# Optimization experiments

Measured on AMD Instinct MI355X. Metric: run time of the kernel, lower is better.

Reference implementation:

```python
import jax, jax.numpy as jnp
import numpy as np

N_NODES = 10000
N_EDGES = 640000
IN_FEATS = 256
H_FEATS = 128
NUM_CLASSES = 64


def _kaiming(key, shape):
    fan_in = shape[1]
    std = np.sqrt(2.0 / fan_in)
    return jax.random.normal(key, shape, dtype=jnp.float32) * std


def setup_inputs() -> dict:
    key = jax.random.key(0)
    ks = jax.random.split(key, 10)
    x = jax.random.normal(ks[0], (N_NODES, IN_FEATS), dtype=jnp.float32)
    edge_index = jax.random.randint(ks[1], (2, N_EDGES), 0, N_NODES, dtype=jnp.int64)
    return {
        "x": x,
        "edge_index": edge_index,
        "W_lin": _kaiming(ks[2], (H_FEATS, IN_FEATS)),
        "b_lin": jnp.zeros((H_FEATS,), jnp.float32),
        "Wl1": _kaiming(ks[3], (H_FEATS, H_FEATS)),
        "bl1": jnp.zeros((H_FEATS,), jnp.float32),
        "Wr1": _kaiming(ks[4], (H_FEATS, H_FEATS)),
        "Wl2": _kaiming(ks[5], (H_FEATS, H_FEATS)),
        "bl2": jnp.zeros((H_FEATS,), jnp.float32),
        "Wr2": _kaiming(ks[6], (H_FEATS, H_FEATS)),
        "W_cls": _kaiming(ks[7], (NUM_CLASSES, H_FEATS)),
    }


def _sage_conv(x, src, dst, Wl, bl, Wr, n_nodes):
    # PyG SAGEConv (mean aggr): out = lin_l(mean_{j->i} x_j) + lin_r(x_i)
    msg = x[src]                                    # [E, H] gather
    agg = jax.ops.segment_sum(msg, dst, num_segments=n_nodes)  # [N, H]
    deg = jax.ops.segment_sum(jnp.ones((src.shape[0],), x.dtype), dst,
                              num_segments=n_nodes)            # [N]
    mean = agg / jnp.maximum(deg, 1.0)[:, None]
    return mean @ Wl.T + bl + x @ Wr.T


def reference(x, edge_index, W_lin, b_lin, Wl1, bl1, Wr1, Wl2, bl2, Wr2, W_cls):
    src, dst = edge_index[0], edge_index[1]
    n = x.shape[0]
    h = jax.nn.relu(x @ W_lin.T + b_lin)            # input projection + relu
    h = _sage_conv(h, src, dst, Wl1, bl1, Wr1, n)   # sage1 (no relu: linear is truthy)
    h = _sage_conv(h, src, dst, Wl2, bl2, Wr2, n)   # sage2
    h = jax.nn.relu(h)
    return h @ W_cls.T                              # weight.mm(x.t()).t()
```

## Files before the change

### kernel.cpp

```cpp
#include <hip/hip_runtime.h>

#define NN 10000
#define HF 128
#define INF_ 256
#define CLS 64
#define NR 8
#define SEG 32
#define CAPT (NR * SEG)
#define NP 10240
#define RT  (NN / 16)
#define LDP (HF + 8)

typedef __attribute__((ext_vector_type(8))) short short8;
typedef __attribute__((ext_vector_type(4))) float f32x4;

__device__ __forceinline__ unsigned short f2bf(float f) {
    unsigned u = __builtin_bit_cast(unsigned, f);
    u = (u + 0x7fffu + ((u >> 16) & 1u)) >> 16;
    return (unsigned short)u;
}
__device__ __forceinline__ float bfbits2f(unsigned u) {
    u <<= 16;
    return __builtin_bit_cast(float, u);
}


template <int K, int NC>
__device__ __forceinline__
void mfma_cols(int row_tile, int col0,
               const unsigned short* __restrict__ A, int lda,
               const unsigned short* __restrict__ W, f32x4* acc) {
    int lane = threadIdx.x & 63;
    int m = lane & 15, quad = lane >> 4;
    const unsigned short* arow = A + (size_t)(row_tile * 16 + m) * lda + quad * 8;
    const short8* bp[NC];
#pragma unroll
    for (int c = 0; c < NC; ++c)
        bp[c] = (const short8*)(W + (size_t)(col0 + c * 16 + m) * K + quad * 8);
#pragma unroll
    for (int k0 = 0; k0 < K; k0 += 32) {
        short8 a = *(const short8*)(arow + k0);
#pragma unroll
        for (int c = 0; c < NC; ++c)
            acc[c] = __builtin_amdgcn_mfma_f32_16x16x32_bf16(a, bp[c][k0 >> 3], acc[c], 0, 0, 0);
    }
}

template <int NC, bool OUT_BF16, bool RELU_OUT, bool HAS_BIAS>
__device__ __forceinline__
void epilogue_n(int row_tile, int col0, int N, const float* __restrict__ bias,
                f32x4* acc, void* __restrict__ out) {
    int lane = threadIdx.x & 63;
    int m = lane & 15, quad = lane >> 4;
#pragma unroll
    for (int c = 0; c < NC; ++c) {
        int colg = col0 + c * 16 + m;
        float bv = HAS_BIAS ? bias[colg] : 0.f;
#pragma unroll
        for (int r = 0; r < 4; ++r) {
            int rowg = row_tile * 16 + quad * 4 + r;
            float v = acc[c][r] + bv;
            if (RELU_OUT) v = fmaxf(v, 0.f);
            if (OUT_BF16) ((unsigned short*)out)[(size_t)rowg * N + colg] = f2bf(v);
            else          ((float*)out)[(size_t)rowg * N + colg] = v;
        }
    }
}

__device__ __forceinline__ short8 pack8(float4 a, float4 b) {
    short8 r;
    r[0] = (short)f2bf(a.x); r[1] = (short)f2bf(a.y);
    r[2] = (short)f2bf(a.z); r[3] = (short)f2bf(a.w);
    r[4] = (short)f2bf(b.x); r[5] = (short)f2bf(b.y);
    r[6] = (short)f2bf(b.z); r[7] = (short)f2bf(b.w);
    return r;
}

__device__ __forceinline__
void gemm1_wave(int row_tile, int col0, const float* __restrict__ x,
                const float* __restrict__ Wlin, const float* __restrict__ blin,
                unsigned short* __restrict__ h0) {
    int lane = threadIdx.x & 63;
    int m = lane & 15, quad = lane >> 4;
    const float* ar = x    + (size_t)(row_tile * 16 + m) * INF_ + quad * 8;
    const float* w0 = Wlin + (size_t)(col0 +  0 + m) * INF_ + quad * 8;
    const float* w1 = Wlin + (size_t)(col0 + 16 + m) * INF_ + quad * 8;
    const float* w2 = Wlin + (size_t)(col0 + 32 + m) * INF_ + quad * 8;
    const float* w3 = Wlin + (size_t)(col0 + 48 + m) * INF_ + quad * 8;
    f32x4 acc[4] = {};
#pragma unroll
    for (int k0 = 0; k0 < INF_; k0 += 32) {
        short8 a  = pack8(*(const float4*)(ar + k0), *(const float4*)(ar + k0 + 4));
        short8 b0 = pack8(*(const float4*)(w0 + k0), *(const float4*)(w0 + k0 + 4));
        short8 b1 = pack8(*(const float4*)(w1 + k0), *(const float4*)(w1 + k0 + 4));
        short8 b2 = pack8(*(const float4*)(w2 + k0), *(const float4*)(w2 + k0 + 4));
        short8 b3 = pack8(*(const float4*)(w3 + k0), *(const float4*)(w3 + k0 + 4));
        acc[0] = __builtin_amdgcn_mfma_f32_16x16x32_bf16(a, b0, acc[0], 0, 0, 0);
        acc[1] = __builtin_amdgcn_mfma_f32_16x16x32_bf16(a, b1, acc[1], 0, 0, 0);
        acc[2] = __builtin_amdgcn_mfma_f32_16x16x32_bf16(a, b2, acc[2], 0, 0, 0);
        acc[3] = __builtin_amdgcn_mfma_f32_16x16x32_bf16(a, b3, acc[3], 0, 0, 0);
    }
    epilogue_n<4, true, true, true>(row_tile, col0, HF, blin, acc, h0);
}

#define GB 313
#define FB 2500
#define CB 288

__global__ __launch_bounds__(256)
void fused_k(const float* __restrict__ x, const float* __restrict__ Wlin,
             const float* __restrict__ blin, unsigned short* __restrict__ h0,
             const int* __restrict__ src, const int* __restrict__ dst,
             int* __restrict__ cnt8, unsigned short* __restrict__ colb, int E,
             const float* __restrict__ Wl1, const float* __restrict__ Wr1,
             const float* __restrict__ Wl2, const float* __restrict__ Wr2,
             const float* __restrict__ Wcls, unsigned short* __restrict__ wb) {
    int b = blockIdx.x;
    if (b < GB) {
        int wave = threadIdx.x >> 6;
        int row_tile = b * 2 + (wave >> 1);
        if (row_tile >= RT) return;
        gemm1_wave(row_tile, (wave & 1) * 64, x, Wlin, blin, h0);
    } else if (b < GB + FB) {
        int r = b & 7;
        int i = (b - GB) * 256 + threadIdx.x;
        if (i < E) {
            int d = dst[i];
            int pos = atomicAdd(&cnt8[r * NP + d], 1);
            if (pos < SEG) colb[(size_t)d * CAPT + r * SEG + pos] = (unsigned short)src[i];
        }
    } else {
        int i = (b - GB - FB) * 256 + threadIdx.x;
        const float* s; int off;
        if      (i < 16384) { s = Wl1;  off = 0; }
        else if (i < 32768) { s = Wr1;  off = 16384; }
        else if (i < 49152) { s = Wl2;  off = 32768; }
        else if (i < 65536) { s = Wr2;  off = 49152; }
        else if (i < 73728) { s = Wcls; off = 65536; }
        else return;
        wb[i] = f2bf(s[i - off]);
    }
}

__device__ __forceinline__
void gather_mean(const unsigned short* __restrict__ h,
                 const int* __restrict__ cnt8, int node,
                 const unsigned short* __restrict__ seg,
                 unsigned short* __restrict__ cols,
                 unsigned short* __restrict__ msrow) {
    int lane = threadIdx.x & 63;
    int q   = lane >> 4;
    int r16 = lane & 15;

    int craw0 = 0;
    if (lane < 8) craw0 = cnt8[lane * NP + node];
    int c0 = craw0 > SEG ? SEG : craw0;
    int off0 = 0, deg = 0, cdeg = 0;
#pragma unroll
    for (int i = 0; i < 8; ++i) {
        int ci = __shfl(c0, i);
        int ri = __shfl(craw0, i);
        if (lane > i) off0 += ci;
        cdeg += ci;
        deg  += ri;
    }
#pragma unroll
    for (int p = 0; p < 4; ++p) {
        int r = 2 * p + (lane >> 5);
        int j = lane & 31;
        unsigned short v = seg[r * SEG + j];
        int cr  = __shfl(c0, r);
        int orr = __shfl(off0, r);
        if (j < cr) cols[orr + j] = v;
    }

    const uint4* __restrict__ hp = (const uint4*)h;
    float a0 = 0.f, a1 = 0.f, a2 = 0.f, a3 = 0.f;
    float a4 = 0.f, a5 = 0.f, a6 = 0.f, a7 = 0.f;
#pragma unroll 4
    for (int e0 = 0; e0 < cdeg; e0 += 4) {
        int e = e0 + q;
        if (e < cdeg) {
            int s = (int)cols[e];
            uint4 v = hp[(size_t)s * 16 + r16];
            a0 += bfbits2f(v.x & 0xffffu); a1 += bfbits2f(v.x >> 16);
            a2 += bfbits2f(v.y & 0xffffu); a3 += bfbits2f(v.y >> 16);
            a4 += bfbits2f(v.z & 0xffffu); a5 += bfbits2f(v.z >> 16);
            a6 += bfbits2f(v.w & 0xffffu); a7 += bfbits2f(v.w >> 16);
        }
    }
    a0 += __shfl_xor(a0, 16); a0 += __shfl_xor(a0, 32);
    a1 += __shfl_xor(a1, 16); a1 += __shfl_xor(a1, 32);
    a2 += __shfl_xor(a2, 16); a2 += __shfl_xor(a2, 32);
    a3 += __shfl_xor(a3, 16); a3 += __shfl_xor(a3, 32);
    a4 += __shfl_xor(a4, 16); a4 += __shfl_xor(a4, 32);
    a5 += __shfl_xor(a5, 16); a5 += __shfl_xor(a5, 32);
    a6 += __shfl_xor(a6, 16); a6 += __shfl_xor(a6, 32);
    a7 += __shfl_xor(a7, 16); a7 += __shfl_xor(a7, 32);
    if (q == 0) {
        float inv = (deg > 0) ? 1.0f / (float)deg : 0.f;
        uint4 o;
        o.x = (unsigned)f2bf(a0 * inv) | ((unsigned)f2bf(a1 * inv) << 16);
        o.y = (unsigned)f2bf(a2 * inv) | ((unsigned)f2bf(a3 * inv) << 16);
        o.z = (unsigned)f2bf(a4 * inv) | ((unsigned)f2bf(a5 * inv) << 16);
        o.w = (unsigned)f2bf(a6 * inv) | ((unsigned)f2bf(a7 * inv) << 16);
        ((uint4*)msrow)[r16] = o;
    }
}

__global__ __launch_bounds__(1024)
void aggfin1_k(const unsigned short* __restrict__ h0, const int* __restrict__ cnt8,
               const unsigned short* __restrict__ colb,
               const unsigned short* __restrict__ Wr, const unsigned short* __restrict__ Wl,
               const float* __restrict__ bias, unsigned short* __restrict__ h1) {
    __shared__ __align__(16) unsigned short ms[16][LDP];
    __shared__ __align__(16) unsigned short colsLds[16][CAPT];
    int wave = threadIdx.x >> 6;
    int node = blockIdx.x * 16 + wave;
    gather_mean(h0, cnt8, node, colb + (size_t)node * CAPT,
                &colsLds[wave][0], &ms[wave][0]);

    f32x4 acc[1] = {};
    if (wave < 8)
        mfma_cols<HF, 1>(blockIdx.x, wave * 16, h0, HF, Wr, acc);
    __syncthreads();
    if (wave < 8) {
        mfma_cols<HF, 1>(0, wave * 16, &ms[0][0], LDP, Wl, acc);
        epilogue_n<1, true, false, true>(blockIdx.x, wave * 16, HF, bias, acc, h1);
    }
}

__global__ __launch_bounds__(1024)
void aggfin2cls_k(const unsigned short* __restrict__ h1, const int* __restrict__ cnt8,
                  const unsigned short* __restrict__ colb,
                  const unsigned short* __restrict__ Wr, const unsigned short* __restrict__ Wl,
                  const float* __restrict__ bias, const unsigned short* __restrict__ Wc,
                  float* __restrict__ out) {
    __shared__ __align__(16) unsigned short ms[16][LDP];
    __shared__ __align__(16) unsigned short h2s[16][LDP];
    __shared__ __align__(16) unsigned short colsLds[16][CAPT];
    int wave = threadIdx.x >> 6;
    int lane = threadIdx.x & 63;
    int m = lane & 15, quad = lane >> 4;
    int node = blockIdx.x * 16 + wave;
    gather_mean(h1, cnt8, node, colb + (size_t)node * CAPT,
                &colsLds[wave][0], &ms[wave][0]);

    f32x4 acc[1] = {};
    if (wave < 8)
        mfma_cols<HF, 1>(blockIdx.x, wave * 16, h1, HF, Wr, acc);
    __syncthreads();
    if (wave < 8) {
        mfma_cols<HF, 1>(0, wave * 16, &ms[0][0], LDP, Wl, acc);
        int colg = wave * 16 + m;
        float bv = bias[colg];
#pragma unroll
        for (int r = 0; r < 4; ++r) {
            float v = acc[0][r] + bv;
            h2s[quad * 4 + r][colg] = f2bf(fmaxf(v, 0.f));
        }
    }
    __syncthreads();
    if (wave < 4) {
        f32x4 cacc[1] = {};
        mfma_cols<HF, 1>(0, wave * 16, &h2s[0][0], LDP, Wc, cacc);
        epilogue_n<1, false, false, false>(blockIdx.x, wave * 16, CLS,
                                           nullptr, cacc, out);
    }
}


extern "C" void kernel_launch(void* const* d_in, const int* in_sizes, int n_in,
                              void* d_out, int out_size, void* d_ws, size_t ws_size,
                              hipStream_t stream) {
    const float* x      = (const float*)d_in[0];
    const int*   ei     = (const int*)d_in[1];
    const float* W_lin  = (const float*)d_in[2];
    const float* b_lin  = (const float*)d_in[3];
    const float* Wl1    = (const float*)d_in[4];
    const float* bl1    = (const float*)d_in[5];
    const float* Wr1    = (const float*)d_in[6];
    const float* Wl2    = (const float*)d_in[7];
    const float* bl2    = (const float*)d_in[8];
    const float* Wr2    = (const float*)d_in[9];
    const float* W_cls  = (const float*)d_in[10];
    float* out = (float*)d_out;

    const int E = in_sizes[1] / 2;
    const int* src = ei;
    const int* dst = ei + E;

    unsigned short* wb  = (unsigned short*)d_ws;
    unsigned short* wbl1 = wb;
    unsigned short* wbr1 = wb + 16384;
    unsigned short* wbl2 = wb + 32768;
    unsigned short* wbr2 = wb + 49152;
    unsigned short* wbc  = wb + 65536;
    unsigned short* h0  = wb + 73728;
    unsigned short* h1  = h0 + (size_t)NN * HF;
    int* cnt8 = (int*)(h1 + (size_t)NN * HF);
    unsigned short* colb = (unsigned short*)(cnt8 + NR * NP);

    hipMemsetAsync(cnt8, 0, NR * NP * sizeof(int), stream);

    fused_k<<<GB + FB + CB, 256, 0, stream>>>(
        x, W_lin, b_lin, h0, src, dst, cnt8, colb, E,
        Wl1, Wr1, Wl2, Wr2, W_cls, wb);

    aggfin1_k<<<RT, 1024, 0, stream>>>(h0, cnt8, colb, wbr1, wbl1, bl1, h1);

    aggfin2cls_k<<<RT, 1024, 0, stream>>>(h1, cnt8, colb, wbr2, wbl2, bl2, wbc, out);
}
```

Before: 160.8 us.

## Shrink aggregation blocks to 8 nodes with 512 threads each

The two aggregate-and-transform kernels now handle 8 nodes per block with 8 waves instead of 16 nodes with 16 waves. All waves now take part in the 16-row MFMA tiles, and only the valid half of the rows is written out. This doubles the block count and removes the 8 waves per block that sat idle during the GEMM phase. In exchange, half of every MFMA tile is wasted, and reads past the last node need padded h0/h1 buffers.

```diff
diff --git a/kernel.cpp b/kernel.cpp
--- a/kernel.cpp
+++ b/kernel.cpp
@@ -9,6 +9,8 @@
 #define CAPT (NR * SEG)
 #define NP 10240
 #define RT  (NN / 16)
+#define NPB 8
+#define NB  (NN / NPB)
 #define LDP (HF + 8)
 
 typedef __attribute__((ext_vector_type(8))) short short8;
@@ -27,12 +29,12 @@
 
 template <int K, int NC>
 __device__ __forceinline__
-void mfma_cols(int row_tile, int col0,
-               const unsigned short* __restrict__ A, int lda,
-               const unsigned short* __restrict__ W, f32x4* acc) {
+void mfma_rows16(int row0, int col0,
+                 const unsigned short* __restrict__ A, int lda,
+                 const unsigned short* __restrict__ W, f32x4* acc) {
     int lane = threadIdx.x & 63;
     int m = lane & 15, quad = lane >> 4;
-    const unsigned short* arow = A + (size_t)(row_tile * 16 + m) * lda + quad * 8;
+    const unsigned short* arow = A + (size_t)(row0 + m) * lda + quad * 8;
     const short8* bp[NC];
 #pragma unroll
     for (int c = 0; c < NC; ++c)
@@ -43,27 +45,6 @@
 #pragma unroll
         for (int c = 0; c < NC; ++c)
             acc[c] = __builtin_amdgcn_mfma_f32_16x16x32_bf16(a, bp[c][k0 >> 3], acc[c], 0, 0, 0);
-    }
-}
-
-template <int NC, bool OUT_BF16, bool RELU_OUT, bool HAS_BIAS>
-__device__ __forceinline__
-void epilogue_n(int row_tile, int col0, int N, const float* __restrict__ bias,
-                f32x4* acc, void* __restrict__ out) {
-    int lane = threadIdx.x & 63;
-    int m = lane & 15, quad = lane >> 4;
-#pragma unroll
-    for (int c = 0; c < NC; ++c) {
-        int colg = col0 + c * 16 + m;
-        float bv = HAS_BIAS ? bias[colg] : 0.f;
-#pragma unroll
-        for (int r = 0; r < 4; ++r) {
-            int rowg = row_tile * 16 + quad * 4 + r;
-            float v = acc[c][r] + bv;
-            if (RELU_OUT) v = fmaxf(v, 0.f);
-            if (OUT_BF16) ((unsigned short*)out)[(size_t)rowg * N + colg] = f2bf(v);
-            else          ((float*)out)[(size_t)rowg * N + colg] = v;
-        }
     }
 }
 
@@ -100,7 +81,16 @@
         acc[2] = __builtin_amdgcn_mfma_f32_16x16x32_bf16(a, b2, acc[2], 0, 0, 0);
         acc[3] = __builtin_amdgcn_mfma_f32_16x16x32_bf16(a, b3, acc[3], 0, 0, 0);
     }
-    epilogue_n<4, true, true, true>(row_tile, col0, HF, blin, acc, h0);
+#pragma unroll
+    for (int c = 0; c < 4; ++c) {
+        int colg = col0 + c * 16 + m;
+        float bv = blin[colg];
+#pragma unroll
+        for (int r = 0; r < 4; ++r) {
+            int rowg = row_tile * 16 + quad * 4 + r;
+            h0[(size_t)rowg * HF + colg] = f2bf(fmaxf(acc[c][r] + bv, 0.f));
+        }
+    }
 }
 
 #define GB 313
@@ -208,29 +198,37 @@
     }
 }
 
-__global__ __launch_bounds__(1024)
+__global__ __launch_bounds__(512)
 void aggfin1_k(const unsigned short* __restrict__ h0, const int* __restrict__ cnt8,
                const unsigned short* __restrict__ colb,
                const unsigned short* __restrict__ Wr, const unsigned short* __restrict__ Wl,
                const float* __restrict__ bias, unsigned short* __restrict__ h1) {
     __shared__ __align__(16) unsigned short ms[16][LDP];
-    __shared__ __align__(16) unsigned short colsLds[16][CAPT];
+    __shared__ __align__(16) unsigned short colsLds[NPB][CAPT];
     int wave = threadIdx.x >> 6;
-    int node = blockIdx.x * 16 + wave;
+    int lane = threadIdx.x & 63;
+    int m = lane & 15, quad = lane >> 4;
+    int row0 = blockIdx.x * NPB;
+    int node = row0 + wave;
     gather_mean(h0, cnt8, node, colb + (size_t)node * CAPT,
                 &colsLds[wave][0], &ms[wave][0]);
 
     f32x4 acc[1] = {};
-    if (wave < 8)
-        mfma_cols<HF, 1>(blockIdx.x, wave * 16, h0, HF, Wr, acc);
+    mfma_rows16<HF, 1>(row0, wave * 16, h0, HF, Wr, acc);
     __syncthreads();
-    if (wave < 8) {
-        mfma_cols<HF, 1>(0, wave * 16, &ms[0][0], LDP, Wl, acc);
-        epilogue_n<1, true, false, true>(blockIdx.x, wave * 16, HF, bias, acc, h1);
-    }
-}
-
-__global__ __launch_bounds__(1024)
+    mfma_rows16<HF, 1>(0, wave * 16, &ms[0][0], LDP, Wl, acc);
+    if (quad < 2) {
+        int colg = wave * 16 + m;
+        float bv = bias[colg];
+#pragma unroll
+        for (int r = 0; r < 4; ++r) {
+            int rowg = row0 + quad * 4 + r;
+            h1[(size_t)rowg * HF + colg] = f2bf(acc[0][r] + bv);
+        }
+    }
+}
+
+__global__ __launch_bounds__(512)
 void aggfin2cls_k(const unsigned short* __restrict__ h1, const int* __restrict__ cnt8,
                   const unsigned short* __restrict__ colb,
                   const unsigned short* __restrict__ Wr, const unsigned short* __restrict__ Wl,
@@ -238,34 +236,39 @@
                   float* __restrict__ out) {
     __shared__ __align__(16) unsigned short ms[16][LDP];
     __shared__ __align__(16) unsigned short h2s[16][LDP];
-    __shared__ __align__(16) unsigned short colsLds[16][CAPT];
+    __shared__ __align__(16) unsigned short colsLds[NPB][CAPT];
     int wave = threadIdx.x >> 6;
     int lane = threadIdx.x & 63;
     int m = lane & 15, quad = lane >> 4;
-    int node = blockIdx.x * 16 + wave;
+    int row0 = blockIdx.x * NPB;
+    int node = row0 + wave;
     gather_mean(h1, cnt8, node, colb + (size_t)node * CAPT,
                 &colsLds[wave][0], &ms[wave][0]);
 
     f32x4 acc[1] = {};
-    if (wave < 8)
-        mfma_cols<HF, 1>(blockIdx.x, wave * 16, h1, HF, Wr, acc);
+    mfma_rows16<HF, 1>(row0, wave * 16, h1, HF, Wr, acc);
     __syncthreads();
-    if (wave < 8) {
-        mfma_cols<HF, 1>(0, wave * 16, &ms[0][0], LDP, Wl, acc);
+    mfma_rows16<HF, 1>(0, wave * 16, &ms[0][0], LDP, Wl, acc);
+    {
         int colg = wave * 16 + m;
         float bv = bias[colg];
 #pragma unroll
         for (int r = 0; r < 4; ++r) {
-            float v = acc[0][r] + bv;
-            h2s[quad * 4 + r][colg] = f2bf(fmaxf(v, 0.f));
+            h2s[quad * 4 + r][colg] = f2bf(fmaxf(acc[0][r] + bv, 0.f));
         }
     }
     __syncthreads();
     if (wave < 4) {
         f32x4 cacc[1] = {};
-        mfma_cols<HF, 1>(0, wave * 16, &h2s[0][0], LDP, Wc, cacc);
-        epilogue_n<1, false, false, false>(blockIdx.x, wave * 16, CLS,
-                                           nullptr, cacc, out);
+        mfma_rows16<HF, 1>(0, wave * 16, &h2s[0][0], LDP, Wc, cacc);
+        if (quad < 2) {
+            int colg = wave * 16 + m;
+#pragma unroll
+            for (int r = 0; r < 4; ++r) {
+                int rowg = row0 + quad * 4 + r;
+                out[(size_t)rowg * CLS + colg] = cacc[0][r];
+            }
+        }
     }
 }
 
@@ -297,8 +300,8 @@
     unsigned short* wbr2 = wb + 49152;
     unsigned short* wbc  = wb + 65536;
     unsigned short* h0  = wb + 73728;
-    unsigned short* h1  = h0 + (size_t)NN * HF;
-    int* cnt8 = (int*)(h1 + (size_t)NN * HF);
+    unsigned short* h1  = h0 + (size_t)(NN + 16) * HF;
+    int* cnt8 = (int*)(h1 + (size_t)(NN + 16) * HF);
     unsigned short* colb = (unsigned short*)(cnt8 + NR * NP);
 
     hipMemsetAsync(cnt8, 0, NR * NP * sizeof(int), stream);
@@ -307,7 +310,7 @@
         x, W_lin, b_lin, h0, src, dst, cnt8, colb, E,
         Wl1, Wr1, Wl2, Wr2, W_cls, wb);
 
-    aggfin1_k<<<RT, 1024, 0, stream>>>(h0, cnt8, colb, wbr1, wbl1, bl1, h1);
-
-    aggfin2cls_k<<<RT, 1024, 0, stream>>>(h1, cnt8, colb, wbr2, wbl2, bl2, wbc, out);
-}
+    aggfin1_k<<<NB, 512, 0, stream>>>(h0, cnt8, colb, wbr1, wbl1, bl1, h1);
+
+    aggfin2cls_k<<<NB, 512, 0, stream>>>(h1, cnt8, colb, wbr2, wbl2, bl2, wbc, out);
+}
```

After: 176.3 us. 1.1x slower.
